# Optimization experiments

Measured on AMD Instinct MI355X. Metric: run time of the kernel, lower is better.

## Reference

```python
import jax, jax.numpy as jnp
import numpy as np

N = 80000    # total nodes
E = 640000   # total edges
B = 800      # graphs in batch
NPG = 100    # nodes per graph
HID = 128
NC = 10
IND = 20     # one-hot degree feature size (torch.eye(20))
EPS = 1e-5


def _gconv(x, src, dst, inv_out, inv_in, W, b):
    # DGL GraphConv, norm='both': D_out^{-1/2} scaling at src, sum-aggregate, D_in^{-1/2} at dst
    m = (x * inv_out[:, None])[src]                      # [E, F]
    agg = jax.ops.segment_sum(m, dst, num_segments=x.shape[0])
    return (agg * inv_in[:, None]) @ W + b


def _bn(x, gamma, beta):
    # BatchNorm1d, training-mode (batch statistics, biased variance)
    mu = x.mean(0)
    var = x.var(0)
    return (x - mu) / jnp.sqrt(var + EPS) * gamma + beta


def setup_inputs():
    key = jax.random.key(0)
    ks = jax.random.split(key, 10)
    # edges constrained within each graph (batched disjoint graphs, as in dgl.batch)
    eg = jax.random.randint(ks[0], (E,), 0, B)
    src = (eg * NPG + jax.random.randint(ks[1], (E,), 0, NPG)).astype(jnp.int32)
    dst = (eg * NPG + jax.random.randint(ks[2], (E,), 0, NPG)).astype(jnp.int32)
    graph_id = (jnp.arange(N) // NPG).astype(jnp.int32)

    def p(k, shape, fan):
        return (jax.random.normal(k, shape, jnp.float32) / np.sqrt(fan)).astype(jnp.float32)

    z = lambda s: jnp.zeros(s, jnp.float32)
    o = lambda s: jnp.ones(s, jnp.float32)
    return dict(
        src=src, dst=dst, graph_id=graph_id,
        W1=p(ks[3], (IND, HID), IND), b1=z((HID,)), g1=o((HID,)), be1=z((HID,)),
        W2=p(ks[4], (HID, HID), HID), b2=z((HID,)), g2=o((HID,)), be2=z((HID,)),
        Wv=p(ks[5], (HID, 1), HID), bv=z((1,)),
        Wd=p(ks[6], (1, HID), 1), bd=z((HID,)),
        Wg=p(ks[7], (HID, HID), HID), bg=z((HID,)), g3=o((HID,)), be3=z((HID,)),
        Wc=p(ks[8], (HID, NC), HID), bc=z((NC,)),
    )


def reference(src, dst, graph_id, W1, b1, g1, be1, W2, b2, g2, be2,
              Wv, bv, Wd, bd, Wg, bg, g3, be3, Wc, bc):
    n = graph_id.shape[0]
    ones_e = jnp.ones(src.shape[0], jnp.float32)
    in_deg = jax.ops.segment_sum(ones_e, dst, num_segments=n)
    out_deg = jax.ops.segment_sum(ones_e, src, num_segments=n)
    inv_in = jax.lax.rsqrt(jnp.maximum(in_deg, 1.0))   # DGL clamps deg min 1
    inv_out = jax.lax.rsqrt(jnp.maximum(out_deg, 1.0))

    # node features: one-hot of in-degree (eye(20)[in_degrees]); clip to valid range
    h = jax.nn.one_hot(jnp.clip(in_deg.astype(jnp.int32), 0, IND - 1), IND, dtype=jnp.float32)
    h = jax.nn.elu(_bn(_gconv(h, src, dst, inv_out, inv_in, W1, b1), g1, be1))  # [N,HID]
    h = jax.nn.elu(_bn(_gconv(h, src, dst, inv_out, inv_in, W2, b2), g2, be2))  # [N,HID]

    v = _gconv(h, src, dst, inv_out, inv_in, Wv, bv)   # [N,1], node weights d
    d = v[:, 0]

    # per-graph ragged matmul: vec_i = d_i^T @ h_i, done as one segment-sum
    vec = jax.ops.segment_sum(d[:, None] * h, graph_id, num_segments=B).reshape(-1)  # [B*HID]
    mean = vec.mean()
    vec = jax.nn.relu(vec - mean) - jax.nn.relu(-vec - mean)   # soft shrink by global mean

    hg = jnp.tanh(vec.reshape(B, HID))
    hg = jnp.tanh(_bn(hg @ Wg + bg, g3, be3))
    return jnp.tanh(hg @ Wc + bc)   # [B, NC] (eval-mode output)
```

## Files before the change

kernel.cpp:

```cpp
#include <hip/hip_runtime.h>
#include <hip/hip_bf16.h>
#include <math.h>

#define N_NODES 80000
#define N_EDGES 640000
#define B_GR 800
#define NPG 100
#define HID 128
#define NC 10
#define IND 20
#define BN_EPS 1e-5f

__global__ void k_degA(const int* __restrict__ src, const int* __restrict__ dst,
                       int* in_deg, int* out_deg, unsigned int* A) {
    int e = blockIdx.x * blockDim.x + threadIdx.x;
    if (e < N_EDGES) {
        int s = src[e], d = dst[e];
        atomicAdd(&in_deg[d], 1);
        atomicAdd(&out_deg[s], 1);
        int g = d / NPG;
        int bidx = g * (NPG * NPG) + (d - g * NPG) * NPG + (s - g * NPG);
        atomicAdd(&A[bidx >> 2], 1u << ((bidx & 3) * 8));
    }
}

__global__ void k_nodeprep(const int* __restrict__ in_deg, const int* __restrict__ out_deg,
                           float* inv_in, float* inv_out, int* idx) {
    int n = blockIdx.x * blockDim.x + threadIdx.x;
    if (n < N_NODES) {
        float fi = (float)in_deg[n];
        float fo = (float)out_deg[n];
        inv_in[n]  = rsqrtf(fmaxf(fi, 1.f));
        inv_out[n] = rsqrtf(fmaxf(fo, 1.f));
        int k = in_deg[n]; if (k > IND - 1) k = IND - 1;
        idx[n] = k;
    }
}

__global__ __launch_bounds__(128) void k_agg20(const unsigned int* __restrict__ A,
                                               const int* __restrict__ idx,
                                               const float* __restrict__ inv_out,
                                               float* __restrict__ agg20) {
    __shared__ float s_io[NPG];
    __shared__ int   s_ix[NPG];
    __shared__ float s_agg[NPG][IND + 1];
    int g = blockIdx.x, gbase = g * NPG, t = threadIdx.x;
    if (t < NPG) { s_io[t] = inv_out[gbase + t]; s_ix[t] = idx[gbase + t]; }
    __syncthreads();
    if (t < NPG) {
#pragma unroll
        for (int k = 0; k < IND; ++k) s_agg[t][k] = 0.f;
        const unsigned int* row = A + g * 2500 + t * 25;
        unsigned int cq[25];
#pragma unroll
        for (int q = 0; q < 25; ++q) cq[q] = row[q];
#pragma unroll
        for (int q = 0; q < 25; ++q) {
            unsigned int c4 = cq[q];
            if (c4 == 0) continue;
#pragma unroll
            for (int b = 0; b < 4; ++b) {
                unsigned int cnt = (c4 >> (8 * b)) & 255u;
                if (cnt) {
                    int s = q * 4 + b;
                    s_agg[t][s_ix[s]] += (float)cnt * s_io[s];
                }
            }
        }
        float* outp = agg20 + (size_t)(gbase + t) * IND;
#pragma unroll
        for (int k = 0; k < IND; ++k) outp[k] = s_agg[t][k];
    }
}

#define MOM_CHUNK 64
__global__ __launch_bounds__(256) void k_mom(const float* __restrict__ agg20,
                                             const float* __restrict__ inv_in,
                                             float* s20, float* Mbuf) {
    __shared__ float rows[MOM_CHUNK * IND];
    __shared__ float w1s[MOM_CHUNK], w2s[MOM_CHUNK];
    int t = threadIdx.x;
    int k = 0, l = 0;
    bool isM = (t < 210), isS = (t >= 210 && t < 230);
    if (isM) {
        int idx = t, kk = 0;
        while (idx >= IND - kk) { idx -= IND - kk; ++kk; }
        k = kk; l = kk + idx;
    } else if (isS) {
        k = t - 210;
    }
    float acc = 0.f;
    for (int c = blockIdx.x; c < N_NODES / MOM_CHUNK; c += gridDim.x) {
        __syncthreads();
        for (int i = t * 4; i < MOM_CHUNK * IND; i += 1024)
            *(float4*)&rows[i] = *(const float4*)&agg20[(size_t)c * MOM_CHUNK * IND + i];
        if (t < MOM_CHUNK) {
            float v = inv_in[c * MOM_CHUNK + t];
            w1s[t] = v; w2s[t] = v * v;
        }
        __syncthreads();
        if (isM) {
            for (int i = 0; i < MOM_CHUNK; ++i)
                acc += w2s[i] * rows[i * IND + k] * rows[i * IND + l];
        } else if (isS) {
            for (int i = 0; i < MOM_CHUNK; ++i)
                acc += w1s[i] * rows[i * IND + k];
        }
    }
    if (isM) atomicAdd(&Mbuf[t], acc);
    else if (isS) atomicAdd(&s20[t - 210], acc);
}

__global__ void k_bn1fin(const float* __restrict__ s20, const float* __restrict__ Mbuf,
                         const float* __restrict__ W1, const float* __restrict__ b1,
                         const float* __restrict__ g1, const float* __restrict__ be1,
                         float* a1, float* c1) {
    __shared__ float sM[210], ss[IND];
    int j = threadIdx.x;
    if (j < 210) sM[j] = Mbuf[j];
    if (j + 128 < 210) sM[j + 128] = Mbuf[j + 128];
    if (j < IND) ss[j] = s20[j];
    __syncthreads();
    float w[IND];
#pragma unroll
    for (int k = 0; k < IND; ++k) w[k] = W1[k * HID + j];
    float tj = 0.f;
#pragma unroll
    for (int k = 0; k < IND; ++k) tj += ss[k] * w[k];
    float q = 0.f;
    int idx = 0;
#pragma unroll
    for (int k = 0; k < IND; ++k) {
        q += sM[idx] * w[k] * w[k]; ++idx;
#pragma unroll
        for (int l = k + 1; l < IND; ++l) { q += 2.f * sM[idx] * w[k] * w[l]; ++idx; }
    }
    float bj = b1[j];
    const float Nf = (float)N_NODES;
    float mean = (tj + Nf * bj) / Nf;
    float ey2  = (q + 2.f * bj * tj + Nf * bj * bj) / Nf;
    float var  = ey2 - mean * mean;
    float aj = g1[j] / sqrtf(var + BN_EPS);
    a1[j] = aj;
    c1[j] = be1[j] - mean * aj;
}

__global__ __launch_bounds__(256) void k_l1f(const float* __restrict__ agg20,
                                             const float* __restrict__ inv_in,
                                             const float* __restrict__ inv_out,
                                             const float* __restrict__ W1,
                                             const float* __restrict__ b1,
                                             const float* __restrict__ a1,
                                             const float* __restrict__ c1,
                                             float* __restrict__ h1s) {
    __shared__ float ws[IND * HID];
    int t = threadIdx.x;
    for (int i = t * 4; i < IND * HID; i += 1024)
        *(float4*)&ws[i] = *(const float4*)&W1[i];
    __syncthreads();
    int tx = t & 15, ty = t >> 4;
    int c0 = tx * 8;
    float4 ba = *(const float4*)(b1 + c0);
    float4 bb = *(const float4*)(b1 + c0 + 4);
    float4 aa = *(const float4*)(a1 + c0);
    float4 ab = *(const float4*)(a1 + c0 + 4);
    float4 ca = *(const float4*)(c1 + c0);
    float4 cb = *(const float4*)(c1 + c0 + 4);

    int row0 = blockIdx.x * 64 + ty * 4;
    const float* xr0 = agg20 + (size_t)row0 * IND;
    const float* xr1 = xr0 + IND;
    const float* xr2 = xr1 + IND;
    const float* xr3 = xr2 + IND;
    float acc[4][8];
#pragma unroll
    for (int r = 0; r < 4; ++r)
#pragma unroll
        for (int c = 0; c < 8; ++c) acc[r][c] = 0.f;

#pragma unroll
    for (int k = 0; k < IND; k += 4) {
        float4 x0 = *(const float4*)(xr0 + k);
        float4 x1 = *(const float4*)(xr1 + k);
        float4 x2 = *(const float4*)(xr2 + k);
        float4 x3 = *(const float4*)(xr3 + k);
#pragma unroll
        for (int kk = 0; kk < 4; ++kk) {
            float4 wa = *(const float4*)&ws[(k + kk) * HID + c0];
            float4 wb = *(const float4*)&ws[(k + kk) * HID + c0 + 4];
            float xk0 = (kk == 0) ? x0.x : (kk == 1) ? x0.y : (kk == 2) ? x0.z : x0.w;
            float xk1 = (kk == 0) ? x1.x : (kk == 1) ? x1.y : (kk == 2) ? x1.z : x1.w;
            float xk2 = (kk == 0) ? x2.x : (kk == 1) ? x2.y : (kk == 2) ? x2.z : x2.w;
            float xk3 = (kk == 0) ? x3.x : (kk == 1) ? x3.y : (kk == 2) ? x3.z : x3.w;
            acc[0][0] += xk0 * wa.x; acc[0][1] += xk0 * wa.y;
            acc[0][2] += xk0 * wa.z; acc[0][3] += xk0 * wa.w;
            acc[0][4] += xk0 * wb.x; acc[0][5] += xk0 * wb.y;
            acc[0][6] += xk0 * wb.z; acc[0][7] += xk0 * wb.w;
            acc[1][0] += xk1 * wa.x; acc[1][1] += xk1 * wa.y;
            acc[1][2] += xk1 * wa.z; acc[1][3] += xk1 * wa.w;
            acc[1][4] += xk1 * wb.x; acc[1][5] += xk1 * wb.y;
            acc[1][6] += xk1 * wb.z; acc[1][7] += xk1 * wb.w;
            acc[2][0] += xk2 * wa.x; acc[2][1] += xk2 * wa.y;
            acc[2][2] += xk2 * wa.z; acc[2][3] += xk2 * wa.w;
            acc[2][4] += xk2 * wb.x; acc[2][5] += xk2 * wb.y;
            acc[2][6] += xk2 * wb.z; acc[2][7] += xk2 * wb.w;
            acc[3][0] += xk3 * wa.x; acc[3][1] += xk3 * wa.y;
            acc[3][2] += xk3 * wa.z; acc[3][3] += xk3 * wa.w;
            acc[3][4] += xk3 * wb.x; acc[3][5] += xk3 * wb.y;
            acc[3][6] += xk3 * wb.z; acc[3][7] += xk3 * wb.w;
        }
    }
    float4 iv = *(const float4*)(inv_in + row0);
    float4 ov = *(const float4*)(inv_out + row0);
#pragma unroll
    for (int r = 0; r < 4; ++r) {
        float ivr = (r == 0) ? iv.x : (r == 1) ? iv.y : (r == 2) ? iv.z : iv.w;
        float ovr = (r == 0) ? ov.x : (r == 1) ? ov.y : (r == 2) ? ov.z : ov.w;
        float y[8];
        y[0] = acc[r][0] * ivr + ba.x; y[1] = acc[r][1] * ivr + ba.y;
        y[2] = acc[r][2] * ivr + ba.z; y[3] = acc[r][3] * ivr + ba.w;
        y[4] = acc[r][4] * ivr + bb.x; y[5] = acc[r][5] * ivr + bb.y;
        y[6] = acc[r][6] * ivr + bb.z; y[7] = acc[r][7] * ivr + bb.w;
        float z[8];
        z[0] = y[0] * aa.x + ca.x; z[1] = y[1] * aa.y + ca.y;
        z[2] = y[2] * aa.z + ca.z; z[3] = y[3] * aa.w + ca.w;
        z[4] = y[4] * ab.x + cb.x; z[5] = y[5] * ab.y + cb.y;
        z[6] = y[6] * ab.z + cb.z; z[7] = y[7] * ab.w + cb.w;
#pragma unroll
        for (int c = 0; c < 8; ++c) {
            float h = z[c] > 0.f ? z[c] : expm1f(z[c]);
            z[c] = h * ovr;
        }
        float* yr = h1s + (size_t)(row0 + r) * HID + c0;
        *(float4*)yr = make_float4(z[0], z[1], z[2], z[3]);
        *(float4*)(yr + 4) = make_float4(z[4], z[5], z[6], z[7]);
    }
}

__global__ __launch_bounds__(512) void k_agg2v5(const unsigned int* __restrict__ A,
                                                const float* __restrict__ h1s,
                                                float* __restrict__ agg2) {
    __shared__ float sh[NPG * HID];
    int t = threadIdx.x;
    int g = blockIdx.x;
    int gbase = g * NPG;

    const float4* srcp = (const float4*)(h1s + (size_t)gbase * HID);
    float4* shp = (float4*)sh;
    for (int i = t; i < (NPG * HID) / 4; i += 512)
        shp[i] = srcp[i];
    __syncthreads();

    int wv = t >> 6, lane = t & 63;
    const unsigned int* Ag = A + g * 2500;
    for (int r = wv; r < NPG; r += 8) {
        const unsigned int* row = Ag + r * 25;
        unsigned int cq[25];
#pragma unroll
        for (int q = 0; q < 25; ++q) cq[q] = row[q];
        float ax = 0.f, ay = 0.f;
#pragma unroll
        for (int q = 0; q < 25; ++q) {
            unsigned int c4 = cq[q];
            if (c4 == 0) continue;
            int sbase = q * 4;
#pragma unroll
            for (int b = 0; b < 4; ++b) {
                unsigned int cnt = (c4 >> (8 * b)) & 255u;
                if (cnt) {
                    float f = (float)cnt;
                    float2 v = *(const float2*)&sh[(sbase + b) * HID + lane * 2];
                    ax += f * v.x; ay += f * v.y;
                }
            }
        }
        *(float2*)(agg2 + (size_t)(gbase + r) * HID + lane * 2) = make_float2(ax, ay);
    }
}

__global__ void k_bnfin(const float* sums, const float* sqs,
                        const float* gamma, const float* beta,
                        float cnt, float* a, float* c) {
    int j = threadIdx.x;
    float mu  = sums[j] / cnt;
    float var = sqs[j] / cnt - mu * mu;
    float aj  = gamma[j] / sqrtf(var + BN_EPS);
    a[j] = aj;
    c[j] = beta[j] - mu * aj;
}

__global__ __launch_bounds__(512) void k_l2v5(const float* __restrict__ xin,
                                              const float* __restrict__ inv_in,
                                              const float* __restrict__ W,
                                              const float* __restrict__ bvec,
                                              float* __restrict__ yout,
                                              float* sums, float* sqs) {
    __shared__ float ws[HID * 64];
    int t = threadIdx.x;
    int tile = blockIdx.x >> 1;
    int half = blockIdx.x & 1;
    int cbase = half * 64;
    for (int i = t; i < HID * 16; i += 512) {
        int k = i >> 4;
        int c4 = (i & 15) << 2;
        *(float4*)&ws[k * 64 + c4] = *(const float4*)&W[k * HID + cbase + c4];
    }
    __syncthreads();

    int tx = t & 15;
    int ty = t >> 4;
    int c0 = tx * 4;
    float4 ba = *(const float4*)(bvec + cbase + c0);
    float csum[4], csq[4];
#pragma unroll
    for (int c = 0; c < 4; ++c) { csum[c] = 0.f; csq[c] = 0.f; }

    int row0 = tile * 128 + ty * 4;
    const float* xr0 = xin + (size_t)row0 * HID;
    const float* xr1 = xr0 + HID;
    const float* xr2 = xr1 + HID;
    const float* xr3 = xr2 + HID;
    float acc[4][4];
#pragma unroll
    for (int r = 0; r < 4; ++r)
#pragma unroll
        for (int c = 0; c < 4; ++c) acc[r][c] = 0.f;

#pragma unroll 4
    for (int k = 0; k < HID; k += 4) {
        float4 x0 = *(const float4*)(xr0 + k);
        float4 x1 = *(const float4*)(xr1 + k);
        float4 x2 = *(const float4*)(xr2 + k);
        float4 x3 = *(const float4*)(xr3 + k);
#pragma unroll
        for (int kk = 0; kk < 4; ++kk) {
            float4 wa = *(const float4*)&ws[(k + kk) * 64 + c0];
            float xk0 = (kk == 0) ? x0.x : (kk == 1) ? x0.y : (kk == 2) ? x0.z : x0.w;
            float xk1 = (kk == 0) ? x1.x : (kk == 1) ? x1.y : (kk == 2) ? x1.z : x1.w;
            float xk2 = (kk == 0) ? x2.x : (kk == 1) ? x2.y : (kk == 2) ? x2.z : x2.w;
            float xk3 = (kk == 0) ? x3.x : (kk == 1) ? x3.y : (kk == 2) ? x3.z : x3.w;
            acc[0][0] += xk0 * wa.x; acc[0][1] += xk0 * wa.y;
            acc[0][2] += xk0 * wa.z; acc[0][3] += xk0 * wa.w;
            acc[1][0] += xk1 * wa.x; acc[1][1] += xk1 * wa.y;
            acc[1][2] += xk1 * wa.z; acc[1][3] += xk1 * wa.w;
            acc[2][0] += xk2 * wa.x; acc[2][1] += xk2 * wa.y;
            acc[2][2] += xk2 * wa.z; acc[2][3] += xk2 * wa.w;
            acc[3][0] += xk3 * wa.x; acc[3][1] += xk3 * wa.y;
            acc[3][2] += xk3 * wa.z; acc[3][3] += xk3 * wa.w;
        }
    }
    float4 iv = *(const float4*)(inv_in + row0);
#pragma unroll
    for (int r = 0; r < 4; ++r) {
        float ivr = (r == 0) ? iv.x : (r == 1) ? iv.y : (r == 2) ? iv.z : iv.w;
        float y0 = acc[r][0] * ivr + ba.x;
        float y1 = acc[r][1] * ivr + ba.y;
        float y2 = acc[r][2] * ivr + ba.z;
        float y3 = acc[r][3] * ivr + ba.w;
        csum[0] += y0; csq[0] += y0 * y0;
        csum[1] += y1; csq[1] += y1 * y1;
        csum[2] += y2; csq[2] += y2 * y2;
        csum[3] += y3; csq[3] += y3 * y3;
        *(float4*)(yout + (size_t)(row0 + r) * HID + cbase + c0) = make_float4(y0, y1, y2, y3);
    }

    __syncthreads();
#pragma unroll
    for (int c = 0; c < 4; ++c) {
        ws[ty * 64 + c0 + c] = csum[c];
        ws[2048 + ty * 64 + c0 + c] = csq[c];
    }
    __syncthreads();
    if (t < 64) {
        float s1 = 0.f, s2 = 0.f;
#pragma unroll
        for (int r = 0; r < 32; ++r) {
            s1 += ws[r * 64 + t];
            s2 += ws[2048 + r * 64 + t];
        }
        atomicAdd(&sums[cbase + t], s1);
        atomicAdd(&sqs[cbase + t], s2);
    }
}

__global__ __launch_bounds__(256) void k_elu2_p(float* buf,
                                                const float* __restrict__ a,
                                                const float* __restrict__ c,
                                                const float* __restrict__ inv_out,
                                                const float* __restrict__ Wv,
                                                float* __restrict__ p) {
    int lane = threadIdx.x & 63;
    int wid = (blockIdx.x * blockDim.x + threadIdx.x) >> 6;
    int nw = (gridDim.x * blockDim.x) >> 6;
    float2 av = *(const float2*)(a + lane * 2);
    float2 cv = *(const float2*)(c + lane * 2);
    float2 wv = *(const float2*)(Wv + lane * 2);
    for (int n = wid; n < N_NODES; n += nw) {
        float2* row = (float2*)(buf + (size_t)n * HID);
        float2 x = row[lane];
        float h0 = x.x * av.x + cv.x; h0 = h0 > 0.f ? h0 : expm1f(h0);
        float h1 = x.y * av.y + cv.y; h1 = h1 > 0.f ? h1 : expm1f(h1);
        row[lane] = make_float2(h0, h1);
        float t = h0 * wv.x + h1 * wv.y;
        for (int off = 32; off; off >>= 1) t += __shfl_down(t, off);
        if (lane == 0) p[n] = t * inv_out[n];
    }
}

__global__ __launch_bounds__(128) void k_dpv2(const unsigned int* __restrict__ A,
                                              const float* __restrict__ p,
                                              const float* __restrict__ inv_in,
                                              const float* __restrict__ bv,
                                              float* __restrict__ dvec) {
    __shared__ float s_p[NPG];
    int g = blockIdx.x, gbase = g * NPG, t = threadIdx.x;
    if (t < NPG) s_p[t] = p[gbase + t];
    __syncthreads();
    if (t < NPG) {
        const unsigned int* row = A + g * 2500 + t * 25;
        unsigned int cq[25];
#pragma unroll
        for (int q = 0; q < 25; ++q) cq[q] = row[q];
        float acc = 0.f;
#pragma unroll
        for (int q = 0; q < 25; ++q) {
            unsigned int c4 = cq[q];
            if (c4 == 0) continue;
#pragma unroll
            for (int b = 0; b < 4; ++b) {
                unsigned int cnt = (c4 >> (8 * b)) & 255u;
                if (cnt) acc += (float)cnt * s_p[q * 4 + b];
            }
        }
        dvec[gbase + t] = acc * inv_in[gbase + t] + bv[0];
    }
}

__global__ __launch_bounds__(128) void k_vec(const float* __restrict__ dvec,
                                             const float* __restrict__ h2,
                                             float* vec, float* meansum) {
    __shared__ float part[2];
    int g = blockIdx.x, j = threadIdx.x;
    int base = g * NPG;
    float acc = 0.f;
    for (int i = 0; i < NPG; ++i)
        acc += dvec[base + i] * h2[(size_t)(base + i) * HID + j];
    vec[g * HID + j] = acc;
    float t = acc;
    for (int off = 32; off; off >>= 1) t += __shfl_down(t, off);
    if ((j & 63) == 0) part[j >> 6] = t;
    __syncthreads();
    if (j == 0) atomicAdd(meansum, part[0] + part[1]);
}

__global__ __launch_bounds__(128) void k_g1(const float* __restrict__ vec,
                                            const float* __restrict__ meansum,
                                            const float* __restrict__ Wg,
                                            const float* __restrict__ bg,
                                            float* y3, float* sums, float* sqs) {
    __shared__ float ws[HID * HID];
    __shared__ float rows[HID];
    int g = blockIdx.x, j = threadIdx.x;
    for (int k = 0; k < HID; ++k) ws[k * HID + j] = Wg[k * HID + j];
    float mean = meansum[0] * (1.f / (B_GR * HID));
    float v = vec[g * HID + j];
    float sh = fmaxf(v - mean, 0.f) - fmaxf(-v - mean, 0.f);
    rows[j] = tanhf(sh);
    __syncthreads();
    float acc = 0.f;
#pragma unroll 8
    for (int k = 0; k < HID; ++k) acc += rows[k] * ws[k * HID + j];
    float y = acc + bg[j];
    y3[g * HID + j] = y;
    atomicAdd(&sums[j], y);
    atomicAdd(&sqs[j], y * y);
}

__global__ __launch_bounds__(128) void k_out(const float* __restrict__ y3,
                                             const float* __restrict__ a,
                                             const float* __restrict__ c,
                                             const float* __restrict__ Wc,
                                             const float* __restrict__ bc,
                                             float* out) {
    __shared__ float hg[HID];
    int g = blockIdx.x, j = threadIdx.x;
    hg[j] = tanhf(y3[g * HID + j] * a[j] + c[j]);
    __syncthreads();
    if (j < NC) {
        float acc = 0.f;
        for (int k = 0; k < HID; ++k) acc += hg[k] * Wc[k * NC + j];
        out[g * NC + j] = tanhf(acc + bc[j]);
    }
}

extern "C" void kernel_launch(void* const* d_in, const int* in_sizes, int n_in,
                              void* d_out, int out_size, void* d_ws, size_t ws_size,
                              hipStream_t stream) {
    const int*   src = (const int*)d_in[0];
    const int*   dst = (const int*)d_in[1];
    const float* W1  = (const float*)d_in[3];
    const float* b1  = (const float*)d_in[4];
    const float* g1  = (const float*)d_in[5];
    const float* be1 = (const float*)d_in[6];
    const float* W2  = (const float*)d_in[7];
    const float* b2  = (const float*)d_in[8];
    const float* g2  = (const float*)d_in[9];
    const float* be2 = (const float*)d_in[10];
    const float* Wv  = (const float*)d_in[11];
    const float* bv  = (const float*)d_in[12];
    const float* Wg  = (const float*)d_in[15];
    const float* bg  = (const float*)d_in[16];
    const float* g3  = (const float*)d_in[17];
    const float* be3 = (const float*)d_in[18];
    const float* Wc  = (const float*)d_in[19];
    const float* bc  = (const float*)d_in[20];
    float* out = (float*)d_out;

    char* ws = (char*)d_ws;
    size_t off = 0;
    auto carve = [&](size_t bytes) -> char* {
        char* pp = ws + off;
        off = (off + bytes + 255) & ~(size_t)255;
        return pp;
    };
    int*   in_deg  = (int*)  carve(N_NODES * 4);
    int*   out_deg = (int*)  carve(N_NODES * 4);
    unsigned int* A = (unsigned int*)carve((size_t)B_GR * NPG * NPG);
    float* stats   = (float*)carve(2048 * 4);
    size_t zbytes = off;
    int*   idx     = (int*)  carve(N_NODES * 4);
    float* inv_in  = (float*)carve(N_NODES * 4);
    float* inv_out = (float*)carve(N_NODES * 4);
    float* pbuf    = (float*)carve(N_NODES * 4);
    float* dvec    = (float*)carve(N_NODES * 4);
    float* vec     = (float*)carve((size_t)B_GR * HID * 4);
    float* y3      = (float*)carve((size_t)B_GR * HID * 4);
    float* agg20   = (float*)carve((size_t)N_NODES * IND * 4);
    float* bufA    = (float*)carve((size_t)N_NODES * HID * 4);
    float* bufB    = (float*)carve((size_t)N_NODES * HID * 4);

    float* sums2 = stats + 0;    float* sq2 = stats + 128;
    float* a2    = stats + 256;  float* c2  = stats + 384;
    float* sums3 = stats + 512;  float* sq3 = stats + 640;
    float* a3    = stats + 768;  float* c3  = stats + 896;
    float* meansum = stats + 1024;
    float* s20   = stats + 1056;
    float* Mbuf  = stats + 1088;
    float* a1    = stats + 1312;
    float* c1    = stats + 1440;

    hipMemsetAsync(d_ws, 0, zbytes, stream);

    k_degA<<<(N_EDGES + 255) / 256, 256, 0, stream>>>(src, dst, in_deg, out_deg, A);
    k_nodeprep<<<(N_NODES + 255) / 256, 256, 0, stream>>>(in_deg, out_deg, inv_in, inv_out, idx);
    k_agg20<<<B_GR, 128, 0, stream>>>(A, idx, inv_out, agg20);
    k_mom<<<320, 256, 0, stream>>>(agg20, inv_in, s20, Mbuf);
    k_bn1fin<<<1, 128, 0, stream>>>(s20, Mbuf, W1, b1, g1, be1, a1, c1);
    k_l1f<<<N_NODES / 64, 256, 0, stream>>>(agg20, inv_in, inv_out, W1, b1, a1, c1, bufA);
    k_agg2v5<<<B_GR, 512, 0, stream>>>(A, bufA, bufB);
    k_l2v5<<<(N_NODES / 128) * 2, 512, 0, stream>>>(bufB, inv_in, W2, b2, bufA, sums2, sq2);
    k_bnfin<<<1, 128, 0, stream>>>(sums2, sq2, g2, be2, (float)N_NODES, a2, c2);
    k_elu2_p<<<1024, 256, 0, stream>>>(bufA, a2, c2, inv_out, Wv, pbuf);
    k_dpv2<<<B_GR, 128, 0, stream>>>(A, pbuf, inv_in, bv, dvec);
    k_vec<<<B_GR, 128, 0, stream>>>(dvec, bufA, vec, meansum);
    k_g1<<<B_GR, 128, 0, stream>>>(vec, meansum, Wg, bg, y3, sums3, sq3);
    k_bnfin<<<1, 128, 0, stream>>>(sums3, sq3, g3, be3, (float)B_GR, a3, c3);
    k_out<<<B_GR, 128, 0, stream>>>(y3, a3, c3, Wc, bc, out);
}
```

Measured before the change: 334.9 us.

## Derive node degrees from the packed adjacency matrix and fuse prep kernels

Removes the per-edge in/out degree atomics and computes in-degree as row sums and out-degree as column sums of the per-graph byte-packed adjacency block. The block is staged in shared memory. The node-prep and one-hot aggregation kernels are merged into one per-graph kernel. This drops 1.28M global atomics, one launch and the idx/degree buffers. In exchange it adds a column-sum loop over shared memory per thread.

New measurement: 287.4 us. 14.2% less time.

```diff
diff --git a/kernel.cpp b/kernel.cpp
--- a/kernel.cpp
+++ b/kernel.cpp
@@ -11,52 +11,59 @@
 #define IND 20
 #define BN_EPS 1e-5f
 
-__global__ void k_degA(const int* __restrict__ src, const int* __restrict__ dst,
-                       int* in_deg, int* out_deg, unsigned int* A) {
+__global__ void k_A(const int* __restrict__ src, const int* __restrict__ dst,
+                    unsigned int* A) {
     int e = blockIdx.x * blockDim.x + threadIdx.x;
     if (e < N_EDGES) {
         int s = src[e], d = dst[e];
-        atomicAdd(&in_deg[d], 1);
-        atomicAdd(&out_deg[s], 1);
         int g = d / NPG;
         int bidx = g * (NPG * NPG) + (d - g * NPG) * NPG + (s - g * NPG);
         atomicAdd(&A[bidx >> 2], 1u << ((bidx & 3) * 8));
     }
 }
 
-__global__ void k_nodeprep(const int* __restrict__ in_deg, const int* __restrict__ out_deg,
-                           float* inv_in, float* inv_out, int* idx) {
-    int n = blockIdx.x * blockDim.x + threadIdx.x;
-    if (n < N_NODES) {
-        float fi = (float)in_deg[n];
-        float fo = (float)out_deg[n];
-        inv_in[n]  = rsqrtf(fmaxf(fi, 1.f));
-        inv_out[n] = rsqrtf(fmaxf(fo, 1.f));
-        int k = in_deg[n]; if (k > IND - 1) k = IND - 1;
-        idx[n] = k;
-    }
-}
-
-__global__ __launch_bounds__(128) void k_agg20(const unsigned int* __restrict__ A,
-                                               const int* __restrict__ idx,
-                                               const float* __restrict__ inv_out,
-                                               float* __restrict__ agg20) {
+__global__ __launch_bounds__(128) void k_prep(const unsigned int* __restrict__ A,
+                                              float* __restrict__ inv_in,
+                                              float* __restrict__ inv_out,
+                                              float* __restrict__ agg20) {
+    __shared__ unsigned int s_A[NPG * 25];
     __shared__ float s_io[NPG];
     __shared__ int   s_ix[NPG];
     __shared__ float s_agg[NPG][IND + 1];
     int g = blockIdx.x, gbase = g * NPG, t = threadIdx.x;
-    if (t < NPG) { s_io[t] = inv_out[gbase + t]; s_ix[t] = idx[gbase + t]; }
-    __syncthreads();
+    const unsigned int* Ag = A + g * 2500;
+    for (int i = t; i < NPG * 25; i += 128) s_A[i] = Ag[i];
+    __syncthreads();
+
     if (t < NPG) {
+        int rsum = 0;
+        const unsigned int* row = &s_A[t * 25];
+#pragma unroll
+        for (int q = 0; q < 25; ++q) {
+            unsigned int c4 = row[q];
+            rsum += (int)((c4 & 255u) + ((c4 >> 8) & 255u) + ((c4 >> 16) & 255u) + (c4 >> 24));
+        }
+        int csum = 0;
+        int wq = t >> 2, sh = (t & 3) * 8;
+#pragma unroll 4
+        for (int r = 0; r < NPG; ++r)
+            csum += (int)((s_A[r * 25 + wq] >> sh) & 255u);
+
+        float io = rsqrtf(fmaxf((float)csum, 1.f));
+        inv_in[gbase + t]  = rsqrtf(fmaxf((float)rsum, 1.f));
+        inv_out[gbase + t] = io;
+        s_io[t] = io;
+        s_ix[t] = rsum > IND - 1 ? IND - 1 : rsum;
+    }
+    __syncthreads();
+
+    if (t < NPG) {
 #pragma unroll
         for (int k = 0; k < IND; ++k) s_agg[t][k] = 0.f;
-        const unsigned int* row = A + g * 2500 + t * 25;
-        unsigned int cq[25];
-#pragma unroll
-        for (int q = 0; q < 25; ++q) cq[q] = row[q];
+        const unsigned int* row = &s_A[t * 25];
 #pragma unroll
         for (int q = 0; q < 25; ++q) {
-            unsigned int c4 = cq[q];
+            unsigned int c4 = row[q];
             if (c4 == 0) continue;
 #pragma unroll
             for (int b = 0; b < 4; ++b) {
@@ -523,12 +530,9 @@
         off = (off + bytes + 255) & ~(size_t)255;
         return pp;
     };
-    int*   in_deg  = (int*)  carve(N_NODES * 4);
-    int*   out_deg = (int*)  carve(N_NODES * 4);
     unsigned int* A = (unsigned int*)carve((size_t)B_GR * NPG * NPG);
     float* stats   = (float*)carve(2048 * 4);
     size_t zbytes = off;
-    int*   idx     = (int*)  carve(N_NODES * 4);
     float* inv_in  = (float*)carve(N_NODES * 4);
     float* inv_out = (float*)carve(N_NODES * 4);
     float* pbuf    = (float*)carve(N_NODES * 4);
@@ -551,9 +555,8 @@
 
     hipMemsetAsync(d_ws, 0, zbytes, stream);
 
-    k_degA<<<(N_EDGES + 255) / 256, 256, 0, stream>>>(src, dst, in_deg, out_deg, A);
-    k_nodeprep<<<(N_NODES + 255) / 256, 256, 0, stream>>>(in_deg, out_deg, inv_in, inv_out, idx);
-    k_agg20<<<B_GR, 128, 0, stream>>>(A, idx, inv_out, agg20);
+    k_A<<<(N_EDGES + 255) / 256, 256, 0, stream>>>(src, dst, A);
+    k_prep<<<B_GR, 128, 0, stream>>>(A, inv_in, inv_out, agg20);
     k_mom<<<320, 256, 0, stream>>>(agg20, inv_in, s20, Mbuf);
     k_bn1fin<<<1, 128, 0, stream>>>(s20, Mbuf, W1, b1, g1, be1, a1, c1);
     k_l1f<<<N_NODES / 64, 256, 0, stream>>>(agg20, inv_in, inv_out, W1, b1, a1, c1, bufA);
```
